# Performance work log

Hardware: AMD Instinct MI355X
Metric: run time of the kernel (lower is better)

The kernel has to match this reference:

```python
import jax, jax.numpy as jnp
import numpy as np

BH, TQ, TK, DK = 64, 1024, 1024, 64  # B_h = B*H = 4*16


def setup_inputs() -> dict:
    key = jax.random.key(0)
    kq, kk, kv, km = jax.random.split(key, 4)
    Q = jax.random.normal(kq, (BH, TQ, DK), dtype=jnp.float32)
    K = jax.random.normal(kk, (BH, TK, DK), dtype=jnp.float32)
    V = jax.random.normal(kv, (BH, TK, DK), dtype=jnp.float32)
    mask = jax.random.randint(km, (BH, TK), 0, 2).astype(bool)  # 2D padding mask
    return {"Q": Q, "K": K, "V": V, "mask": mask, "head_ablation": 3, "num_heads": 16}


def reference(Q, K, V, mask, head_ablation, num_heads):
    B_h, T_q, d_k = Q.shape
    T_k = K.shape[1]
    # scores = Q K^T / sqrt(d_k), full [B_h, T_q, T_k] matrix as in the original
    scores = jnp.einsum('bqd,bkd->bqk', Q, K) / jnp.sqrt(jnp.asarray(d_k, Q.dtype))
    # 2D mask -> broadcast over query dim (mask.unsqueeze(1).expand in torch)
    m = jnp.broadcast_to(mask[:, None, :], (B_h, T_q, T_k))
    scores = jnp.where(m, scores, jnp.finfo(scores.dtype).min)
    weights = jax.nn.softmax(scores, axis=-1)
    # zero rows whose mask is fully off (torch fully_masked branch)
    fully_masked = m.sum(axis=-1, keepdims=True) == 0
    weights = jnp.where(fully_masked, jnp.zeros((), weights.dtype), weights)
    # head ablation: zero attention weights of one head
    B = B_h // num_heads
    weights = (weights.reshape(B, num_heads, T_q, T_k)
                      .at[:, head_ablation].set(0.0)
                      .reshape(B_h, T_q, T_k))
    # dropout_p = 0.0 -> identity
    output = jnp.einsum('bqk,bkd->bqd', weights, V)
    return (output, weights)
```

## Files before the change

### kernel.cpp

```cpp
#include <hip/hip_runtime.h>
#include <hip/hip_bf16.h>
#include <cfloat>
#include <cstdint>

#define BH 64
#define TQ 1024
#define TK 1024
#define DK 64
#define WSTR 1032

typedef __attribute__((ext_vector_type(8))) short short8;
typedef __attribute__((ext_vector_type(4))) short short4v;
typedef __attribute__((ext_vector_type(4))) float f32x4;

__device__ __forceinline__ short bf16r(float f) {
    union { float f; unsigned u; } x; x.f = f;
    unsigned r = x.u + 0x7fffu + ((x.u >> 16) & 1u);
    return (short)(r >> 16);
}

__device__ __forceinline__ float bf2f(short s) {
    union { unsigned u; float f; } x; x.u = ((unsigned)(unsigned short)s) << 16;
    return x.f;
}

__device__ __forceinline__ short8 load8_bf16(const float* p) {
    float4 a = *(const float4*)p;
    float4 b = *(const float4*)(p + 4);
    short8 r;
    r[0] = bf16r(a.x); r[1] = bf16r(a.y); r[2] = bf16r(a.z); r[3] = bf16r(a.w);
    r[4] = bf16r(b.x); r[5] = bf16r(b.y); r[6] = bf16r(b.z); r[7] = bf16r(b.w);
    return r;
}

__global__ __launch_bounds__(256) void pack_k(const float* __restrict__ K,
                                              short* __restrict__ Kp) {
    const int g = blockIdx.x * 256 + threadIdx.x;
    const int lane = g & 63, half = (g >> 6) & 1, tg = (g >> 7) & 63, b = g >> 13;
    const int key = tg * 16 + (lane & 15);
    const int d = half * 32 + (lane >> 4) * 8;
    short8 o = load8_bf16(K + ((size_t)b * TK + key) * DK + d);
    *(short8*)(Kp + (size_t)g * 8) = o;
}

__global__ __launch_bounds__(256) void pack_v(const float* __restrict__ V,
                                              short* __restrict__ Vp) {
    __shared__ short tile[64 * 72];
    const int tid = threadIdx.x;
    const int k0 = blockIdx.x * 64, b = blockIdx.y;

    #pragma unroll
    for (int it = 0; it < 4; ++it) {
        int lin = it * 256 + tid;
        int kl = lin >> 4;
        int d0 = (lin & 15) * 4;
        float4 v = *(const float4*)(V + ((size_t)b * TK + k0 + kl) * DK + d0);
        short4v o; o[0] = bf16r(v.x); o[1] = bf16r(v.y); o[2] = bf16r(v.z); o[3] = bf16r(v.w);
        *(short4v*)&tile[kl * 72 + d0] = o;
    }
    __syncthreads();
    #pragma unroll
    for (int it = 0; it < 4; ++it) {
        int lin = it * 256 + tid;
        int d = lin & 63;
        int kg = (lin >> 6) * 4;
        int key = k0 + kg;
        int kk = key >> 5;
        int quad = (kg >> 3) & 3, j0 = kg & 7;
        int lane = (d & 15) + 16 * quad, t = d >> 4;
        short4v o;
        #pragma unroll
        for (int i = 0; i < 4; ++i) o[i] = tile[(kg + i) * 72 + d];
        *(short4v*)&Vp[((((size_t)b * 32 + kk) * 4 + t) * 512) + lane * 8 + j0] = o;
    }
}

__global__ __launch_bounds__(256, 4) void attn_fused(const float* __restrict__ Q,
                                                     const short* __restrict__ Kp,
                                                     const short* __restrict__ Vp,
                                                     const void* __restrict__ mask,
                                                     float* __restrict__ Wout,
                                                     float* __restrict__ O,
                                                     const int* __restrict__ ha_p,
                                                     const int* __restrict__ nh_p) {
    __shared__ short Wlds[16 * WSTR];
    __shared__ float red2[16][4];
    __shared__ int mflags[2];

    const int tid = threadIdx.x;
    const int id = blockIdx.x;
    const int b = id & 63, qt = id >> 6;
    const int q0 = qt * 16;

    if ((b % nh_p[0]) == ha_p[0]) {
        const float4 z = {0.f, 0.f, 0.f, 0.f};
        #pragma unroll
        for (int i = 0; i < 16; ++i)
            *(float4*)&Wout[((size_t)b * TQ + q0 + i) * TK + tid * 4] = z;
        *(float4*)&O[((size_t)b * TQ + q0 + (tid >> 4)) * DK + (tid & 15) * 4] = z;
        return;
    }

    if (tid == 0) { mflags[0] = 0; mflags[1] = 0; }
    __syncthreads();
    {
        unsigned v = ((const unsigned*)mask)[tid];
        bool f32pat = (v == 0x3f800000u);
        bool u8pat = (v > 1u) && !f32pat;
        unsigned long long bu = __ballot(u8pat);
        unsigned long long bf = __ballot(f32pat);
        if ((tid & 63) == 0) {
            if (bu) atomicOr(&mflags[0], 1);
            if (bf) atomicOr(&mflags[1], 1);
        }
    }
    __syncthreads();
    const int mode = mflags[0] ? 0 : (mflags[1] ? 2 : 1);

    const int lane = tid & 63, wave = tid >> 6;
    const int m = lane & 15, quad = lane >> 4;
    const int kw = wave * 256;

    const float* qrow = Q + ((size_t)b * TQ + q0 + m) * DK + quad * 8;
    short8 a0 = load8_bf16(qrow);
    short8 a1 = load8_bf16(qrow + 32);

    const uint8_t* m8  = (const uint8_t*)mask + (size_t)b * TK + kw;
    const int*     m32 = (const int*)mask     + (size_t)b * TK + kw;
    const float*   mfp = (const float*)mask   + (size_t)b * TK + kw;

    const short* kpb = Kp + ((size_t)b * 64 + wave * 16) * 1024 + lane * 8;
    float sum[4] = {0.f, 0.f, 0.f, 0.f};
    #pragma unroll 4
    for (int t = 0; t < 16; ++t) {
        short8 b0 = *(const short8*)(kpb + t * 1024);
        short8 b1 = *(const short8*)(kpb + t * 1024 + 512);
        f32x4 c = {0.f, 0.f, 0.f, 0.f};
        c = __builtin_amdgcn_mfma_f32_16x16x32_bf16(a0, b0, c, 0, 0, 0);
        c = __builtin_amdgcn_mfma_f32_16x16x32_bf16(a1, b1, c, 0, 0, 0);
        const int col = t * 16 + m;
        const bool mk = (mode == 0) ? (m8[col] != 0)
                      : (mode == 1) ? (m32[col] != 0)
                                    : (mfp[col] != 0.0f);
        #pragma unroll
        for (int r = 0; r < 4; ++r) {
            float p = mk ? __expf(fminf(c[r] * 0.125f, 60.f)) : 0.f;
            sum[r] += p;
            Wlds[(quad * 4 + r) * WSTR + kw + col] = bf16r(p);
        }
    }
    #pragma unroll
    for (int r = 0; r < 4; ++r) {
        float v = sum[r];
        v += __shfl_xor(v, 1); v += __shfl_xor(v, 2);
        v += __shfl_xor(v, 4); v += __shfl_xor(v, 8);
        if (m == 0) red2[quad * 4 + r][wave] = v;
    }
    __syncthreads();

    #pragma unroll 4
    for (int i = 0; i < 16; ++i) {
        float4 s4 = *(float4*)red2[i];
        float tot = (s4.x + s4.y) + (s4.z + s4.w);
        float inv = (tot == 0.f) ? 0.f : 1.0f / tot;
        short4v p4 = *(short4v*)&Wlds[i * WSTR + tid * 4];
        float4 w;
        w.x = bf2f(p4[0]) * inv; w.y = bf2f(p4[1]) * inv;
        w.z = bf2f(p4[2]) * inv; w.w = bf2f(p4[3]) * inv;
        *(float4*)&Wout[((size_t)b * TQ + q0 + i) * TK + tid * 4] = w;
    }

    float inv4[4];
    #pragma unroll
    for (int r = 0; r < 4; ++r) {
        float4 s4 = *(float4*)red2[quad * 4 + r];
        float tot = (s4.x + s4.y) + (s4.z + s4.w);
        inv4[r] = (tot == 0.f) ? 0.f : 1.0f / tot;
    }
    const short* vpb = Vp + (((size_t)b * 32) * 4 + wave) * 512 + lane * 8;
    f32x4 oacc = {0.f, 0.f, 0.f, 0.f};
    #pragma unroll 8
    for (int kk = 0; kk < 32; ++kk) {
        short8 a = *(const short8*)&Wlds[m * WSTR + kk * 32 + quad * 8];
        short8 bb = *(const short8*)(vpb + (size_t)kk * 2048);
        oacc = __builtin_amdgcn_mfma_f32_16x16x32_bf16(a, bb, oacc, 0, 0, 0);
    }
    #pragma unroll
    for (int r = 0; r < 4; ++r)
        O[((size_t)b * TQ + q0 + quad * 4 + r) * DK + wave * 16 + m] = oacc[r] * inv4[r];
}

extern "C" void kernel_launch(void* const* d_in, const int* in_sizes, int n_in,
                              void* d_out, int out_size, void* d_ws, size_t ws_size,
                              hipStream_t stream) {
    const float* Q    = (const float*)d_in[0];
    const float* Kmat = (const float*)d_in[1];
    const float* V    = (const float*)d_in[2];
    const void*  mask = d_in[3];
    const int*   ha   = (const int*)d_in[4];
    const int*   nh   = (const int*)d_in[5];

    float* out     = (float*)d_out;
    float* weights = out + (size_t)BH * TQ * DK;

    short* Kp = (short*)d_ws;
    short* Vp = Kp + (size_t)BH * TK * DK;

    pack_k<<<dim3(BH * TK * DK / 8 / 256), 256, 0, stream>>>(Kmat, Kp);
    pack_v<<<dim3(TK / 64, BH), 256, 0, stream>>>(V, Vp);
    attn_fused<<<dim3(TQ / 16 * BH), 256, 0, stream>>>(Q, Kp, Vp, mask, weights, out, ha, nh);
}
```

Baseline: 378.4 us.

## Merge pack kernels, precompute float mask, transpose QK MFMA for vector LDS stores

Merges the K and V packing kernels into one launch that also converts the mask into a float 0/1 array, so the attention kernel no longer repeats mask format detection in every block. The QK MFMA operands are swapped, so each lane holds four consecutive keys of one query row. This lets it store its four bf16 probabilities with a single vector LDS write, multiply by a vectorized float4 mask load, and reduce row sums with two shuffles instead of four. It costs extra workspace for the float mask and relies on the workspace being large enough.

Result: no change. 376.1 us (-0.6%).

```diff
diff --git a/kernel.cpp b/kernel.cpp
--- a/kernel.cpp
+++ b/kernel.cpp
@@ -33,59 +33,92 @@
     return r;
 }
 
-__global__ __launch_bounds__(256) void pack_k(const float* __restrict__ K,
-                                              short* __restrict__ Kp) {
-    const int g = blockIdx.x * 256 + threadIdx.x;
-    const int lane = g & 63, half = (g >> 6) & 1, tg = (g >> 7) & 63, b = g >> 13;
-    const int key = tg * 16 + (lane & 15);
-    const int d = half * 32 + (lane >> 4) * 8;
-    short8 o = load8_bf16(K + ((size_t)b * TK + key) * DK + d);
-    *(short8*)(Kp + (size_t)g * 8) = o;
-}
-
-__global__ __launch_bounds__(256) void pack_v(const float* __restrict__ V,
-                                              short* __restrict__ Vp) {
+__global__ __launch_bounds__(256) void pack_kv(const float* __restrict__ K,
+                                               const float* __restrict__ V,
+                                               const void* __restrict__ mask,
+                                               short* __restrict__ Kp,
+                                               short* __restrict__ Vp,
+                                               float* __restrict__ Mf) {
     __shared__ short tile[64 * 72];
+    __shared__ int mflags[2];
     const int tid = threadIdx.x;
-    const int k0 = blockIdx.x * 64, b = blockIdx.y;
-
-    #pragma unroll
-    for (int it = 0; it < 4; ++it) {
-        int lin = it * 256 + tid;
-        int kl = lin >> 4;
-        int d0 = (lin & 15) * 4;
-        float4 v = *(const float4*)(V + ((size_t)b * TK + k0 + kl) * DK + d0);
-        short4v o; o[0] = bf16r(v.x); o[1] = bf16r(v.y); o[2] = bf16r(v.z); o[3] = bf16r(v.w);
-        *(short4v*)&tile[kl * 72 + d0] = o;
-    }
-    __syncthreads();
-    #pragma unroll
-    for (int it = 0; it < 4; ++it) {
-        int lin = it * 256 + tid;
-        int d = lin & 63;
-        int kg = (lin >> 6) * 4;
-        int key = k0 + kg;
-        int kk = key >> 5;
-        int quad = (kg >> 3) & 3, j0 = kg & 7;
-        int lane = (d & 15) + 16 * quad, t = d >> 4;
-        short4v o;
-        #pragma unroll
-        for (int i = 0; i < 4; ++i) o[i] = tile[(kg + i) * 72 + d];
-        *(short4v*)&Vp[((((size_t)b * 32 + kk) * 4 + t) * 512) + lane * 8 + j0] = o;
+    const int bid = blockIdx.x;
+
+    if (bid < 2048) {
+        const int g = bid * 256 + tid;
+        const int lane = g & 63, half = (g >> 6) & 1, tg = (g >> 7) & 63, b = g >> 13;
+        const int key = tg * 16 + (lane & 15);
+        const int d = half * 32 + (lane >> 4) * 8;
+        short8 o = load8_bf16(K + ((size_t)b * TK + key) * DK + d);
+        *(short8*)(Kp + (size_t)g * 8) = o;
+    } else if (bid < 3072) {
+        const int vb = bid - 2048;
+        const int k0 = (vb & 15) * 64, b = vb >> 4;
+        #pragma unroll
+        for (int it = 0; it < 4; ++it) {
+            int lin = it * 256 + tid;
+            int kl = lin >> 4;
+            int d0 = (lin & 15) * 4;
+            float4 v = *(const float4*)(V + ((size_t)b * TK + k0 + kl) * DK + d0);
+            short4v o; o[0] = bf16r(v.x); o[1] = bf16r(v.y); o[2] = bf16r(v.z); o[3] = bf16r(v.w);
+            *(short4v*)&tile[kl * 72 + d0] = o;
+        }
+        __syncthreads();
+        #pragma unroll
+        for (int it = 0; it < 4; ++it) {
+            int lin = it * 256 + tid;
+            int d = lin & 63;
+            int kg = (lin >> 6) * 4;
+            int key = k0 + kg;
+            int kk = key >> 5;
+            int quad = (kg >> 3) & 3, j0 = kg & 7;
+            int lane = (d & 15) + 16 * quad, t = d >> 4;
+            short4v o;
+            #pragma unroll
+            for (int i = 0; i < 4; ++i) o[i] = tile[(kg + i) * 72 + d];
+            *(short4v*)&Vp[((((size_t)b * 32 + kk) * 4 + t) * 512) + lane * 8 + j0] = o;
+        }
+    } else {
+        const int b = bid - 3072;
+        if (tid == 0) { mflags[0] = 0; mflags[1] = 0; }
+        __syncthreads();
+        {
+            unsigned v = ((const unsigned*)mask)[tid];
+            bool f32pat = (v == 0x3f800000u);
+            bool u8pat = (v > 1u) && !f32pat;
+            unsigned long long bu = __ballot(u8pat);
+            unsigned long long bf = __ballot(f32pat);
+            if ((tid & 63) == 0) {
+                if (bu) atomicOr(&mflags[0], 1);
+                if (bf) atomicOr(&mflags[1], 1);
+            }
+        }
+        __syncthreads();
+        const int mode = mflags[0] ? 0 : (mflags[1] ? 2 : 1);
+        const uint8_t* m8  = (const uint8_t*)mask + (size_t)b * TK;
+        const int*     m32 = (const int*)mask     + (size_t)b * TK;
+        const float*   mfp = (const float*)mask   + (size_t)b * TK;
+        #pragma unroll
+        for (int i = 0; i < 4; ++i) {
+            int col = i * 256 + tid;
+            bool mk = (mode == 0) ? (m8[col] != 0)
+                    : (mode == 1) ? (m32[col] != 0)
+                                  : (mfp[col] != 0.0f);
+            Mf[(size_t)b * TK + col] = mk ? 1.0f : 0.0f;
+        }
     }
 }
 
 __global__ __launch_bounds__(256, 4) void attn_fused(const float* __restrict__ Q,
                                                      const short* __restrict__ Kp,
                                                      const short* __restrict__ Vp,
-                                                     const void* __restrict__ mask,
+                                                     const float* __restrict__ Mf,
                                                      float* __restrict__ Wout,
                                                      float* __restrict__ O,
                                                      const int* __restrict__ ha_p,
                                                      const int* __restrict__ nh_p) {
     __shared__ short Wlds[16 * WSTR];
     __shared__ float red2[16][4];
-    __shared__ int mflags[2];
 
     const int tid = threadIdx.x;
     const int id = blockIdx.x;
@@ -101,22 +134,6 @@
         return;
     }
 
-    if (tid == 0) { mflags[0] = 0; mflags[1] = 0; }
-    __syncthreads();
-    {
-        unsigned v = ((const unsigned*)mask)[tid];
-        bool f32pat = (v == 0x3f800000u);
-        bool u8pat = (v > 1u) && !f32pat;
-        unsigned long long bu = __ballot(u8pat);
-        unsigned long long bf = __ballot(f32pat);
-        if ((tid & 63) == 0) {
-            if (bu) atomicOr(&mflags[0], 1);
-            if (bf) atomicOr(&mflags[1], 1);
-        }
-    }
-    __syncthreads();
-    const int mode = mflags[0] ? 0 : (mflags[1] ? 2 : 1);
-
     const int lane = tid & 63, wave = tid >> 6;
     const int m = lane & 15, quad = lane >> 4;
     const int kw = wave * 256;
@@ -125,37 +142,29 @@
     short8 a0 = load8_bf16(qrow);
     short8 a1 = load8_bf16(qrow + 32);
 
-    const uint8_t* m8  = (const uint8_t*)mask + (size_t)b * TK + kw;
-    const int*     m32 = (const int*)mask     + (size_t)b * TK + kw;
-    const float*   mfp = (const float*)mask   + (size_t)b * TK + kw;
-
+    const float* mfp = Mf + (size_t)b * TK + kw;
     const short* kpb = Kp + ((size_t)b * 64 + wave * 16) * 1024 + lane * 8;
-    float sum[4] = {0.f, 0.f, 0.f, 0.f};
+    float sum = 0.f;
     #pragma unroll 4
     for (int t = 0; t < 16; ++t) {
-        short8 b0 = *(const short8*)(kpb + t * 1024);
-        short8 b1 = *(const short8*)(kpb + t * 1024 + 512);
+        short8 k0 = *(const short8*)(kpb + t * 1024);
+        short8 k1 = *(const short8*)(kpb + t * 1024 + 512);
         f32x4 c = {0.f, 0.f, 0.f, 0.f};
-        c = __builtin_amdgcn_mfma_f32_16x16x32_bf16(a0, b0, c, 0, 0, 0);
-        c = __builtin_amdgcn_mfma_f32_16x16x32_bf16(a1, b1, c, 0, 0, 0);
-        const int col = t * 16 + m;
-        const bool mk = (mode == 0) ? (m8[col] != 0)
-                      : (mode == 1) ? (m32[col] != 0)
-                                    : (mfp[col] != 0.0f);
+        c = __builtin_amdgcn_mfma_f32_16x16x32_bf16(k0, a0, c, 0, 0, 0);
+        c = __builtin_amdgcn_mfma_f32_16x16x32_bf16(k1, a1, c, 0, 0, 0);
+        float4 mf = *(const float4*)(mfp + t * 16 + quad * 4);
+        short4v pw;
         #pragma unroll
         for (int r = 0; r < 4; ++r) {
-            float p = mk ? __expf(fminf(c[r] * 0.125f, 60.f)) : 0.f;
-            sum[r] += p;
-            Wlds[(quad * 4 + r) * WSTR + kw + col] = bf16r(p);
-        }
-    }
-    #pragma unroll
-    for (int r = 0; r < 4; ++r) {
-        float v = sum[r];
-        v += __shfl_xor(v, 1); v += __shfl_xor(v, 2);
-        v += __shfl_xor(v, 4); v += __shfl_xor(v, 8);
-        if (m == 0) red2[quad * 4 + r][wave] = v;
-    }
+            float p = ((const float*)&mf)[r] * __expf(fminf(c[r] * 0.125f, 60.f));
+            sum += p;
+            pw[r] = bf16r(p);
+        }
+        *(short4v*)&Wlds[m * WSTR + kw + t * 16 + quad * 4] = pw;
+    }
+    sum += __shfl_xor(sum, 16);
+    sum += __shfl_xor(sum, 32);
+    if (quad == 0) red2[m][wave] = sum;
     __syncthreads();
 
     #pragma unroll 4
@@ -205,8 +214,8 @@
 
     short* Kp = (short*)d_ws;
     short* Vp = Kp + (size_t)BH * TK * DK;
-
-    pack_k<<<dim3(BH * TK * DK / 8 / 256), 256, 0, stream>>>(Kmat, Kp);
-    pack_v<<<dim3(TK / 64, BH), 256, 0, stream>>>(V, Vp);
-    attn_fused<<<dim3(TQ / 16 * BH), 256, 0, stream>>>(Q, Kp, Vp, mask, weights, out, ha, nh);
-}
+    float* Mf = (float*)(Vp + (size_t)BH * TK * DK);
+
+    pack_kv<<<dim3(3136), 256, 0, stream>>>(Kmat, V, mask, Kp, Vp, Mf);
+    attn_fused<<<dim3(TQ / 16 * BH), 256, 0, stream>>>(Q, Kp, Vp, Mf, weights, out, ha, nh);
+}
```
